# Performance work log

Measured on AMD Instinct MI355X. Metric: run time of the kernel, lower is better.

Reference implementation:

```python
import jax, jax.numpy as jnp
import numpy as np

LAMBDA_SCR = 0.015
LAMBDA_IFD = 0.015


def setup_inputs() -> dict:
    key = jax.random.key(0)
    k = jax.random.split(key, 5)
    pred = jax.random.normal(k[0], (32, 1000), dtype=jnp.float32)
    feat0 = jax.random.normal(k[1], (32, 64, 128, 128), dtype=jnp.float32)
    feat1 = jax.random.normal(k[2], (32, 128, 64, 64), dtype=jnp.float32)
    feat2 = jax.random.normal(k[3], (32, 256, 32, 32), dtype=jnp.float32)  # teacher
    target = jax.random.randint(k[4], (32,), 0, 1000, dtype=jnp.int64)
    return {"pred": pred, "feat0": feat0, "feat1": feat1, "feat2": feat2, "target": target}


def _adaptive_avg_pool2d(x, out_hw):
    # Exact-multiple adaptive average pool (matches torch for integer ratios).
    B, C, H, W = x.shape
    Ho, Wo = out_hw
    if Ho >= H:
        x = jnp.repeat(x, Ho // H, axis=2)  # replication upsample
    else:
        x = x.reshape(B, C, Ho, H // Ho, W).mean(axis=3)
    if Wo >= W:
        x = jnp.repeat(x, Wo // W, axis=3)
    else:
        x = x.reshape(B, C, x.shape[2], Wo, W // Wo).mean(axis=4)
    return x


def _random_channel_selection(feat, target_channels, key):
    C = feat.shape[1]
    if C == target_channels:
        return feat
    idx = jax.random.permutation(key, C)[:target_channels]
    return feat[:, idx, :, :]


def _ifd_loss(feat):
    B, C, H, W = feat.shape
    if C < 2:
        return jnp.float32(0.0)
    # L2 norm per channel -> descending sort of channel indices
    norms = jnp.linalg.norm(feat.reshape(B, C, H * W), axis=-1)  # [B, C]
    idx = jnp.argsort(-norms, axis=1)                            # [B, C]
    half = C // 2
    strong = jnp.take_along_axis(feat, idx[:, :half, None, None], axis=1)
    weak = jnp.take_along_axis(feat, idx[:, half:2 * half, None, None], axis=1)
    A_strong = jax.nn.sigmoid(strong.mean(axis=1))  # [B, H, W]
    A_weak = jax.nn.sigmoid(weak.mean(axis=1))
    # sum_b mean_hw(diff^2) / B == mean over all elements
    return jnp.mean((A_weak - jax.lax.stop_gradient(A_strong)) ** 2)


def reference(pred, feat0, feat1, feat2, target):
    logp = jax.nn.log_softmax(pred, axis=-1)
    l_main = -jnp.mean(jnp.take_along_axis(logp, target[:, None], axis=1))

    features = [feat0, feat1, feat2]
    teacher = features[-1]
    students = features[:-1]

    sel_key = jax.random.key(42)  # fixed keys stand in for torch.randperm
    l_scr = jnp.float32(0.0)
    for i, student in enumerate(students):
        t_down = _adaptive_avg_pool2d(teacher, student.shape[2:])
        min_C = min(teacher.shape[1], student.shape[1])
        ks, kt = jax.random.split(jax.random.fold_in(sel_key, i))
        s_aligned = _random_channel_selection(student, min_C, ks)
        t_aligned = _random_channel_selection(t_down, min_C, kt)
        l_scr = l_scr + jnp.mean((s_aligned - jax.lax.stop_gradient(t_aligned)) ** 2)
    l_scr = l_scr / len(students)

    l_ifd = jnp.float32(0.0)
    for feat in features:
        l_ifd = l_ifd + _ifd_loss(feat)
    l_ifd = l_ifd / len(features)

    total = l_main + LAMBDA_SCR * l_scr + LAMBDA_IFD * l_ifd
    return (total, l_main, l_scr, l_ifd)
```

## Files before the change

### kernel.cpp

```cpp
#include <hip/hip_runtime.h>
#include <stdint.h>
#include <math.h>

#define NB 32

__device__ __forceinline__ void tf_block(uint32_t k0, uint32_t k1, uint32_t& x0, uint32_t& x1) {
  uint32_t k2 = 0x1BD11BDAu ^ k0 ^ k1;
  x0 += k0; x1 += k1;
#define TFR(r) { x0 += x1; x1 = (x1 << r) | (x1 >> (32 - r)); x1 ^= x0; }
  TFR(13) TFR(15) TFR(26) TFR(6)
  x0 += k1; x1 += k2 + 1u;
  TFR(17) TFR(29) TFR(16) TFR(24)
  x0 += k2; x1 += k0 + 2u;
  TFR(13) TFR(15) TFR(26) TFR(6)
  x0 += k0; x1 += k1 + 3u;
  TFR(17) TFR(29) TFR(16) TFR(24)
  x0 += k1; x1 += k2 + 4u;
  TFR(13) TFR(15) TFR(26) TFR(6)
  x0 += k2; x1 += k0 + 5u;
#undef TFR
}

__device__ __forceinline__ float sigmoidf(float x) { return 1.0f / (1.0f + expf(-x)); }

__device__ __forceinline__ float block_reduce(float v, float* red) {
  __syncthreads();
  int lane = threadIdx.x & 63, wv = threadIdx.x >> 6;
  for (int o = 32; o > 0; o >>= 1) v += __shfl_down(v, o, 64);
  if (lane == 0) red[wv] = v;
  __syncthreads();
  float r = 0.f;
  if (threadIdx.x == 0) r = red[0] + red[1] + red[2] + red[3];
  return r;
}

__global__ __launch_bounds__(256) void k0_perm(int* idx0, int* idx1, float* ws) {
  __shared__ uint32_t sub[2][2];
  __shared__ uint32_t bits[2][256];
  int t = threadIdx.x;
  for (int i = t; i < 384; i += 256) ws[i] = 0.0f;
  if (t == 0) {
    for (int i = 0; i < 2; ++i) {
      uint32_t f0 = 0u, f1 = (uint32_t)i;
      tf_block(0u, 42u, f0, f1);
      uint32_t a0 = 0u, a1 = 2u; tf_block(f0, f1, a0, a1);
      uint32_t b0 = 1u, b1 = 3u; tf_block(f0, f1, b0, b1);
      uint32_t kt0 = a1, kt1 = b1;
      uint32_t c0 = 0u, c1 = 2u; tf_block(kt0, kt1, c0, c1);
      uint32_t d0 = 1u, d1 = 3u; tf_block(kt0, kt1, d0, d1);
      sub[i][0] = c1; sub[i][1] = d1;
    }
  }
  __syncthreads();
  if (t < 128) {
    for (int i = 0; i < 2; ++i) {
      uint32_t x0 = (uint32_t)t, x1 = (uint32_t)(t + 128);
      tf_block(sub[i][0], sub[i][1], x0, x1);
      bits[i][t] = x0; bits[i][t + 128] = x1;
    }
  }
  __syncthreads();
  for (int i = 0; i < 2; ++i) {
    uint32_t mine = bits[i][t];
    int rank = 0;
    for (int k = 0; k < 256; ++k) {
      uint32_t v = bits[i][k];
      rank += (v < mine) || (v == mine && k < t);
    }
    int lim = (i == 0) ? 64 : 128;
    if (rank < lim) { (i == 0 ? idx0 : idx1)[rank] = t; }
  }
}

template<int C, int HW, int LOGW, int SHIFT, bool STUDENT>
__device__ __forceinline__ void pass1_work(const float* __restrict__ feat,
                                           const float* __restrict__ teacher,
                                           const int* __restrict__ tidx,
                                           float* __restrict__ normsq,
                                           float* __restrict__ scr_slots,
                                           int bc, float* tpl, float* red) {
  if constexpr (STUDENT) {
    int b = bc / C, c = bc % C;
    int tc = tidx[c];
    ((float4*)tpl)[threadIdx.x] =
        ((const float4*)(teacher + ((size_t)b * 256 + tc) * 1024))[threadIdx.x];
    __syncthreads();
  }
  const float4* plane = (const float4*)(feat + (size_t)bc * HW);
  float ssq = 0.f, scr = 0.f;
  for (int p = threadIdx.x; p < HW / 4; p += 256) {
    float4 v = plane[p];
    ssq += v.x * v.x + v.y * v.y + v.z * v.z + v.w * v.w;
    if constexpr (STUDENT) {
      int pix = p * 4;
      int h = pix >> LOGW;
      int w = pix & ((1 << LOGW) - 1);
      int th = h >> SHIFT;
      if constexpr (SHIFT == 2) {
        float tv = tpl[th * 32 + (w >> 2)];
        float dx = v.x - tv, dy = v.y - tv, dz = v.z - tv, dw = v.w - tv;
        scr += dx * dx + dy * dy + dz * dz + dw * dw;
      } else {
        int tw = w >> 1;
        float t0 = tpl[th * 32 + tw], t1 = tpl[th * 32 + tw + 1];
        float dx = v.x - t0, dy = v.y - t0, dz = v.z - t1, dw = v.w - t1;
        scr += dx * dx + dy * dy + dz * dz + dw * dw;
      }
    }
  }
  float r = block_reduce(ssq, red);
  if (threadIdx.x == 0) normsq[bc] = r;
  if constexpr (STUDENT) {
    float r2 = block_reduce(scr, red);
    if (threadIdx.x == 0) atomicAdd(&scr_slots[bc & 63], r2);
  }
}

__global__ __launch_bounds__(256) void k1_pass1(
    const float* __restrict__ f0, const float* __restrict__ f1, const float* __restrict__ f2,
    const int* __restrict__ idx0, const int* __restrict__ idx1,
    float* __restrict__ ns0, float* __restrict__ ns1, float* __restrict__ ns2,
    float* __restrict__ scr0_s, float* __restrict__ scr1_s) {
  __shared__ float tpl[1024];
  __shared__ float red[8];
  int bid = blockIdx.x;
  if (bid < 2048)       pass1_work<64, 16384, 7, 2, true >(f0, f2, idx0, ns0, scr0_s, bid,        tpl, red);
  else if (bid < 6144)  pass1_work<128, 4096, 6, 1, true >(f1, f2, idx1, ns1, scr1_s, bid - 2048, tpl, red);
  else                  pass1_work<256, 1024, 5, 0, false>(f2, nullptr, nullptr, ns2, nullptr, bid - 6144, tpl, red);
}

template<int C>
__device__ __forceinline__ void rank_work(const float* __restrict__ normsq,
                                          float* __restrict__ flags, int b, float* nm) {
  for (int c = threadIdx.x; c < C; c += 256) nm[c] = sqrtf(normsq[b * C + c]);
  __syncthreads();
  for (int c = threadIdx.x; c < C; c += 256) {
    float mine = nm[c];
    int rank = 0;
    for (int k = 0; k < C; ++k) {
      float v = nm[k];
      rank += (v > mine) || (v == mine && k < c);
    }
    flags[b * C + c] = (rank < C / 2) ? 1.0f : 0.0f;
  }
}

__device__ __forceinline__ void main_work(const float* __restrict__ pred,
                                          const int* __restrict__ target,
                                          float* acc, int b, float* sh) {
  int t = threadIdx.x;
  const float* row = pred + b * 1000;
  float m = -INFINITY;
  for (int j = t; j < 1000; j += 256) m = fmaxf(m, row[j]);
  sh[t] = m; __syncthreads();
  for (int s = 128; s > 0; s >>= 1) { if (t < s) sh[t] = fmaxf(sh[t], sh[t + s]); __syncthreads(); }
  m = sh[0]; __syncthreads();
  float e = 0.f;
  for (int j = t; j < 1000; j += 256) e += expf(row[j] - m);
  sh[t] = e; __syncthreads();
  for (int s = 128; s > 0; s >>= 1) { if (t < s) sh[t] += sh[t + s]; __syncthreads(); }
  if (t == 0) atomicAdd(acc, (logf(sh[0]) + m - row[target[b]]) * (1.0f / 32.0f));
}

__global__ __launch_bounds__(256) void k2_rank_main(
    const float* __restrict__ ns0, const float* __restrict__ ns1, const float* __restrict__ ns2,
    float* __restrict__ fl0, float* __restrict__ fl1, float* __restrict__ fl2,
    const float* __restrict__ pred, const int* __restrict__ target, float* main_acc) {
  __shared__ float sh[256];
  int bid = blockIdx.x;
  if (bid < 32)       rank_work<64 >(ns0, fl0, bid,      sh);
  else if (bid < 64)  rank_work<128>(ns1, fl1, bid - 32, sh);
  else if (bid < 96)  rank_work<256>(ns2, fl2, bid - 64, sh);
  else                main_work(pred, target, main_acc, bid - 96, sh);
}

template<int C, int HW>
__device__ __forceinline__ void pass2_vec4_work(const float* __restrict__ feat,
                                                const float* __restrict__ flags,
                                                float* __restrict__ slots, float inv_half,
                                                int bid, float* fl, float* red) {
  const int nchunk = HW / 1024;
  int b = bid / nchunk, chunk = bid % nchunk;
  for (int c = threadIdx.x; c < C; c += 256) fl[c] = flags[b * C + c];
  __syncthreads();
  const float* base = feat + (size_t)b * C * HW + (size_t)chunk * 1024;
  float4 tot = {0, 0, 0, 0}, str = {0, 0, 0, 0};
  for (int c = 0; c < C; ++c) {
    float4 v = ((const float4*)(base + (size_t)c * HW))[threadIdx.x];
    float f = fl[c];
    tot.x += v.x; tot.y += v.y; tot.z += v.z; tot.w += v.w;
    str.x = fmaf(v.x, f, str.x); str.y = fmaf(v.y, f, str.y);
    str.z = fmaf(v.z, f, str.z); str.w = fmaf(v.w, f, str.w);
  }
  float s = 0.f, d;
  d = sigmoidf((tot.x - str.x) * inv_half) - sigmoidf(str.x * inv_half); s += d * d;
  d = sigmoidf((tot.y - str.y) * inv_half) - sigmoidf(str.y * inv_half); s += d * d;
  d = sigmoidf((tot.z - str.z) * inv_half) - sigmoidf(str.z * inv_half); s += d * d;
  d = sigmoidf((tot.w - str.w) * inv_half) - sigmoidf(str.w * inv_half); s += d * d;
  float r = block_reduce(s, red);
  if (threadIdx.x == 0) atomicAdd(&slots[bid & 63], r);
}

__device__ __forceinline__ void pass2_feat2_work(const float* __restrict__ feat,
                                                 const float* __restrict__ flags,
                                                 float* __restrict__ slots, int bid,
                                                 float* fl, float* stot, float* sstr, float* red) {
  int b = bid >> 5, h = bid & 31;
  fl[threadIdx.x] = flags[b * 256 + threadIdx.x];
  __syncthreads();
  int w = threadIdx.x & 31;
  int cl = threadIdx.x >> 5;
  const float* base = feat + (size_t)b * 256 * 1024 + h * 32 + w;
  float tot = 0.f, str = 0.f;
  for (int cg = 0; cg < 32; ++cg) {
    int c = cg * 8 + cl;
    float v = base[(size_t)c * 1024];
    tot += v; str = fmaf(v, fl[c], str);
  }
  stot[threadIdx.x] = tot; sstr[threadIdx.x] = str;
  __syncthreads();
  float s = 0.f;
  if (threadIdx.x < 32) {
    float T = 0.f, S = 0.f;
    for (int k = 0; k < 8; ++k) { T += stot[k * 32 + threadIdx.x]; S += sstr[k * 32 + threadIdx.x]; }
    const float ih = 1.0f / 128.0f;
    float d = sigmoidf((T - S) * ih) - sigmoidf(S * ih);
    s = d * d;
  }
  float r = block_reduce(s, red);
  if (threadIdx.x == 0) atomicAdd(&slots[bid & 63], r);
}

__global__ __launch_bounds__(256) void k3_pass2(
    const float* __restrict__ f0, const float* __restrict__ f1, const float* __restrict__ f2,
    const float* __restrict__ fl0, const float* __restrict__ fl1, const float* __restrict__ fl2,
    float* __restrict__ ifd0_s, float* __restrict__ ifd1_s, float* __restrict__ ifd2_s) {
  __shared__ float fl[256];
  __shared__ float s1[256];
  __shared__ float s2[256];
  __shared__ float red[8];
  int bid = blockIdx.x;
  if (bid < 512)      pass2_vec4_work<64, 16384>(f0, fl0, ifd0_s, 1.0f / 32.0f, bid, fl, red);
  else if (bid < 640) pass2_vec4_work<128, 4096>(f1, fl1, ifd1_s, 1.0f / 64.0f, bid - 512, fl, red);
  else                pass2_feat2_work(f2, fl2, ifd2_s, bid - 640, fl, s1, s2, red);
}

__global__ void k4_finalize(const float* __restrict__ ws, float* __restrict__ out) {
  float scr0 = 0.f, scr1 = 0.f, ifd0 = 0.f, ifd1 = 0.f, ifd2 = 0.f;
  for (int i = 0; i < 64; ++i) {
    scr0 += ws[i];       scr1 += ws[64 + i];
    ifd0 += ws[128 + i]; ifd1 += ws[192 + i]; ifd2 += ws[256 + i];
  }
  float l_main = ws[320];
  scr0 *= (1.0f / (32.0f * 64.0f * 128.0f * 128.0f));
  scr1 *= (1.0f / (32.0f * 128.0f * 64.0f * 64.0f));
  float l_scr = 0.5f * (scr0 + scr1);
  ifd0 *= (1.0f / (32.0f * 128.0f * 128.0f));
  ifd1 *= (1.0f / (32.0f * 64.0f * 64.0f));
  ifd2 *= (1.0f / (32.0f * 32.0f * 32.0f));
  float l_ifd = (ifd0 + ifd1 + ifd2) * (1.0f / 3.0f);
  float total = l_main + 0.015f * l_scr + 0.015f * l_ifd;
  out[0] = total; out[1] = l_main; out[2] = l_scr; out[3] = l_ifd;
}

extern "C" void kernel_launch(void* const* d_in, const int* in_sizes, int n_in,
                              void* d_out, int out_size, void* d_ws, size_t ws_size,
                              hipStream_t stream) {
  (void)in_sizes; (void)n_in; (void)out_size; (void)ws_size;
  const float* pred   = (const float*)d_in[0];
  const float* feat0  = (const float*)d_in[1];
  const float* feat1  = (const float*)d_in[2];
  const float* feat2  = (const float*)d_in[3];
  const int*   target = (const int*)d_in[4];
  float* out = (float*)d_out;

  float* ws = (float*)d_ws;
  float* scr0_s = ws;
  float* scr1_s = ws + 64;
  float* ifd0_s = ws + 128;
  float* ifd1_s = ws + 192;
  float* ifd2_s = ws + 256;
  float* main_a = ws + 320;
  int*   idx0 = (int*)(ws + 384);
  int*   idx1 = idx0 + 64;
  float* ns0  = (float*)(idx1 + 128);
  float* ns1  = ns0 + 2048;
  float* ns2  = ns1 + 4096;
  float* fl0  = ns2 + 8192;
  float* fl1  = fl0 + 2048;
  float* fl2  = fl1 + 4096;

  k0_perm<<<1, 256, 0, stream>>>(idx0, idx1, ws);
  k1_pass1<<<14336, 256, 0, stream>>>(feat0, feat1, feat2, idx0, idx1, ns0, ns1, ns2, scr0_s, scr1_s);
  k2_rank_main<<<128, 256, 0, stream>>>(ns0, ns1, ns2, fl0, fl1, fl2, pred, target, main_a);
  k3_pass2<<<1664, 256, 0, stream>>>(feat0, feat1, feat2, fl0, fl1, fl2, ifd0_s, ifd1_s, ifd2_s);
  k4_finalize<<<1, 1, 0, stream>>>(ws, out);
}
```

Measured before the change: 337.0 us.

## Assign per-wave work units and replace block reductions with wave reductions

The norm/SCR pass and the IFD pass now give each 64-lane wave its own plane or chunk for the smaller feature maps, so one 256-thread block covers four units and the grids shrink. Block-level reductions, with their two barriers and shared-memory round trip, become wave shuffles plus a single barrier or none, and loops get fixed trip counts with unrolling. The aim is to cut barrier and launch overhead and raise memory-level parallelism on these bandwidth-bound passes. The trade-off is more atomics per block and a larger shared-memory footprint, which can lower occupancy.

New measurement: 339.1 us. No clear change (+0.6%).

```diff
diff --git a/kernel.cpp b/kernel.cpp
--- a/kernel.cpp
+++ b/kernel.cpp
@@ -23,15 +23,9 @@
 
 __device__ __forceinline__ float sigmoidf(float x) { return 1.0f / (1.0f + expf(-x)); }
 
-__device__ __forceinline__ float block_reduce(float v, float* red) {
-  __syncthreads();
-  int lane = threadIdx.x & 63, wv = threadIdx.x >> 6;
+__device__ __forceinline__ float wave_reduce(float v) {
   for (int o = 32; o > 0; o >>= 1) v += __shfl_down(v, o, 64);
-  if (lane == 0) red[wv] = v;
-  __syncthreads();
-  float r = 0.f;
-  if (threadIdx.x == 0) r = red[0] + red[1] + red[2] + red[3];
-  return r;
+  return v;
 }
 
 __global__ __launch_bounds__(256) void k0_perm(int* idx0, int* idx1, float* ws) {
@@ -72,61 +66,83 @@
   }
 }
 
-template<int C, int HW, int LOGW, int SHIFT, bool STUDENT>
-__device__ __forceinline__ void pass1_work(const float* __restrict__ feat,
-                                           const float* __restrict__ teacher,
-                                           const int* __restrict__ tidx,
-                                           float* __restrict__ normsq,
-                                           float* __restrict__ scr_slots,
-                                           int bc, float* tpl, float* red) {
-  if constexpr (STUDENT) {
-    int b = bc / C, c = bc % C;
-    int tc = tidx[c];
-    ((float4*)tpl)[threadIdx.x] =
-        ((const float4*)(teacher + ((size_t)b * 256 + tc) * 1024))[threadIdx.x];
-    __syncthreads();
-  }
-  const float4* plane = (const float4*)(feat + (size_t)bc * HW);
-  float ssq = 0.f, scr = 0.f;
-  for (int p = threadIdx.x; p < HW / 4; p += 256) {
-    float4 v = plane[p];
-    ssq += v.x * v.x + v.y * v.y + v.z * v.z + v.w * v.w;
-    if constexpr (STUDENT) {
-      int pix = p * 4;
-      int h = pix >> LOGW;
-      int w = pix & ((1 << LOGW) - 1);
-      int th = h >> SHIFT;
-      if constexpr (SHIFT == 2) {
-        float tv = tpl[th * 32 + (w >> 2)];
-        float dx = v.x - tv, dy = v.y - tv, dz = v.z - tv, dw = v.w - tv;
-        scr += dx * dx + dy * dy + dz * dz + dw * dw;
-      } else {
-        int tw = w >> 1;
-        float t0 = tpl[th * 32 + tw], t1 = tpl[th * 32 + tw + 1];
-        float dx = v.x - t0, dy = v.y - t0, dz = v.z - t1, dw = v.w - t1;
-        scr += dx * dx + dy * dy + dz * dz + dw * dw;
-      }
-    }
-  }
-  float r = block_reduce(ssq, red);
-  if (threadIdx.x == 0) normsq[bc] = r;
-  if constexpr (STUDENT) {
-    float r2 = block_reduce(scr, red);
-    if (threadIdx.x == 0) atomicAdd(&scr_slots[bc & 63], r2);
-  }
-}
-
 __global__ __launch_bounds__(256) void k1_pass1(
     const float* __restrict__ f0, const float* __restrict__ f1, const float* __restrict__ f2,
     const int* __restrict__ idx0, const int* __restrict__ idx1,
     float* __restrict__ ns0, float* __restrict__ ns1, float* __restrict__ ns2,
     float* __restrict__ scr0_s, float* __restrict__ scr1_s) {
-  __shared__ float tpl[1024];
+  __shared__ float tpl[4096];
   __shared__ float red[8];
   int bid = blockIdx.x;
-  if (bid < 2048)       pass1_work<64, 16384, 7, 2, true >(f0, f2, idx0, ns0, scr0_s, bid,        tpl, red);
-  else if (bid < 6144)  pass1_work<128, 4096, 6, 1, true >(f1, f2, idx1, ns1, scr1_s, bid - 2048, tpl, red);
-  else                  pass1_work<256, 1024, 5, 0, false>(f2, nullptr, nullptr, ns2, nullptr, bid - 6144, tpl, red);
+  int lane = threadIdx.x & 63, wv = threadIdx.x >> 6;
+  if (bid < 2048) {
+    int b = bid >> 6, c = bid & 63;
+    int tc = idx0[c];
+    ((float4*)tpl)[threadIdx.x] = ((const float4*)(f2 + ((size_t)b * 256 + tc) * 1024))[threadIdx.x];
+    __syncthreads();
+    const float4* plane = (const float4*)(f0 + (size_t)bid * 16384);
+    float ssq = 0.f, scr = 0.f;
+#pragma unroll 8
+    for (int it = 0; it < 16; ++it) {
+      int p = (wv * 16 + it) * 64 + lane;
+      float4 v = plane[p];
+      int pix = p * 4, h = pix >> 7, w = pix & 127;
+      float tv = tpl[(h >> 2) * 32 + (w >> 2)];
+      ssq += v.x * v.x + v.y * v.y + v.z * v.z + v.w * v.w;
+      float dx = v.x - tv, dy = v.y - tv, dz = v.z - tv, dw = v.w - tv;
+      scr += dx * dx + dy * dy + dz * dz + dw * dw;
+    }
+    ssq = wave_reduce(ssq); scr = wave_reduce(scr);
+    if (lane == 0) { red[wv] = ssq; red[4 + wv] = scr; }
+    __syncthreads();
+    if (threadIdx.x == 0) {
+      ns0[bid] = red[0] + red[1] + red[2] + red[3];
+      atomicAdd(&scr0_s[bid & 63], red[4] + red[5] + red[6] + red[7]);
+    }
+  } else if (bid < 3072) {
+    int unit = ((bid - 2048) << 2) + wv;
+    int b = unit >> 7, c = unit & 127;
+    int tc = idx1[c];
+    const float4* tp = (const float4*)(f2 + ((size_t)b * 256 + tc) * 1024);
+#pragma unroll
+    for (int it = 0; it < 4; ++it)
+      ((float4*)tpl)[(wv << 8) + it * 64 + lane] = tp[it * 64 + lane];
+    __syncthreads();
+    const float* mytpl = tpl + (wv << 10);
+    const float4* plane = (const float4*)(f1 + (size_t)unit * 4096);
+    float ssq = 0.f, scr = 0.f;
+#pragma unroll 8
+    for (int it = 0; it < 16; ++it) {
+      int p = it * 64 + lane;
+      float4 v = plane[p];
+      int pix = p * 4, h = pix >> 6, w = pix & 63;
+      int tb = (h >> 1) * 32 + (w >> 1);
+      float t0 = mytpl[tb], t1 = mytpl[tb + 1];
+      ssq += v.x * v.x + v.y * v.y + v.z * v.z + v.w * v.w;
+      float dx = v.x - t0, dy = v.y - t0, dz = v.z - t1, dw = v.w - t1;
+      scr += dx * dx + dy * dy + dz * dz + dw * dw;
+    }
+    ssq = wave_reduce(ssq); scr = wave_reduce(scr);
+    if (lane == 0) {
+      ns1[unit] = ssq;
+      atomicAdd(&scr1_s[unit & 63], scr);
+    }
+  } else {
+    int u4 = ((bid - 3072) << 2) + wv;
+    int p0 = u4 << 2;
+#pragma unroll
+    for (int j = 0; j < 4; ++j) {
+      const float4* plane = (const float4*)(f2 + (size_t)(p0 + j) * 1024);
+      float ssq = 0.f;
+#pragma unroll
+      for (int it = 0; it < 4; ++it) {
+        float4 v = plane[it * 64 + lane];
+        ssq += v.x * v.x + v.y * v.y + v.z * v.z + v.w * v.w;
+      }
+      ssq = wave_reduce(ssq);
+      if (lane == 0) ns2[p0 + j] = ssq;
+    }
+  }
 }
 
 template<int C>
@@ -174,75 +190,78 @@
   else                main_work(pred, target, main_acc, bid - 96, sh);
 }
 
-template<int C, int HW>
-__device__ __forceinline__ void pass2_vec4_work(const float* __restrict__ feat,
-                                                const float* __restrict__ flags,
-                                                float* __restrict__ slots, float inv_half,
-                                                int bid, float* fl, float* red) {
-  const int nchunk = HW / 1024;
-  int b = bid / nchunk, chunk = bid % nchunk;
-  for (int c = threadIdx.x; c < C; c += 256) fl[c] = flags[b * C + c];
-  __syncthreads();
-  const float* base = feat + (size_t)b * C * HW + (size_t)chunk * 1024;
-  float4 tot = {0, 0, 0, 0}, str = {0, 0, 0, 0};
-  for (int c = 0; c < C; ++c) {
-    float4 v = ((const float4*)(base + (size_t)c * HW))[threadIdx.x];
-    float f = fl[c];
-    tot.x += v.x; tot.y += v.y; tot.z += v.z; tot.w += v.w;
-    str.x = fmaf(v.x, f, str.x); str.y = fmaf(v.y, f, str.y);
-    str.z = fmaf(v.z, f, str.z); str.w = fmaf(v.w, f, str.w);
-  }
-  float s = 0.f, d;
-  d = sigmoidf((tot.x - str.x) * inv_half) - sigmoidf(str.x * inv_half); s += d * d;
-  d = sigmoidf((tot.y - str.y) * inv_half) - sigmoidf(str.y * inv_half); s += d * d;
-  d = sigmoidf((tot.z - str.z) * inv_half) - sigmoidf(str.z * inv_half); s += d * d;
-  d = sigmoidf((tot.w - str.w) * inv_half) - sigmoidf(str.w * inv_half); s += d * d;
-  float r = block_reduce(s, red);
-  if (threadIdx.x == 0) atomicAdd(&slots[bid & 63], r);
-}
-
-__device__ __forceinline__ void pass2_feat2_work(const float* __restrict__ feat,
-                                                 const float* __restrict__ flags,
-                                                 float* __restrict__ slots, int bid,
-                                                 float* fl, float* stot, float* sstr, float* red) {
-  int b = bid >> 5, h = bid & 31;
-  fl[threadIdx.x] = flags[b * 256 + threadIdx.x];
-  __syncthreads();
-  int w = threadIdx.x & 31;
-  int cl = threadIdx.x >> 5;
-  const float* base = feat + (size_t)b * 256 * 1024 + h * 32 + w;
-  float tot = 0.f, str = 0.f;
-  for (int cg = 0; cg < 32; ++cg) {
-    int c = cg * 8 + cl;
-    float v = base[(size_t)c * 1024];
-    tot += v; str = fmaf(v, fl[c], str);
-  }
-  stot[threadIdx.x] = tot; sstr[threadIdx.x] = str;
-  __syncthreads();
-  float s = 0.f;
-  if (threadIdx.x < 32) {
-    float T = 0.f, S = 0.f;
-    for (int k = 0; k < 8; ++k) { T += stot[k * 32 + threadIdx.x]; S += sstr[k * 32 + threadIdx.x]; }
-    const float ih = 1.0f / 128.0f;
-    float d = sigmoidf((T - S) * ih) - sigmoidf(S * ih);
-    s = d * d;
-  }
-  float r = block_reduce(s, red);
-  if (threadIdx.x == 0) atomicAdd(&slots[bid & 63], r);
-}
-
 __global__ __launch_bounds__(256) void k3_pass2(
     const float* __restrict__ f0, const float* __restrict__ f1, const float* __restrict__ f2,
     const float* __restrict__ fl0, const float* __restrict__ fl1, const float* __restrict__ fl2,
     float* __restrict__ ifd0_s, float* __restrict__ ifd1_s, float* __restrict__ ifd2_s) {
-  __shared__ float fl[256];
-  __shared__ float s1[256];
-  __shared__ float s2[256];
-  __shared__ float red[8];
+  __shared__ float fls[1024];
   int bid = blockIdx.x;
-  if (bid < 512)      pass2_vec4_work<64, 16384>(f0, fl0, ifd0_s, 1.0f / 32.0f, bid, fl, red);
-  else if (bid < 640) pass2_vec4_work<128, 4096>(f1, fl1, ifd1_s, 1.0f / 64.0f, bid - 512, fl, red);
-  else                pass2_feat2_work(f2, fl2, ifd2_s, bid - 640, fl, s1, s2, red);
+  int lane = threadIdx.x & 63, wv = threadIdx.x >> 6;
+  if (bid < 512) {
+    int unit = (bid << 2) + wv;
+    int b = unit >> 6, chunk = unit & 63;
+    float* fl = fls + (wv << 8);
+    fl[lane] = fl0[(b << 6) + lane];
+    const float* base = f0 + (size_t)b * 64 * 16384 + (size_t)chunk * 256;
+    float4 tot = {0, 0, 0, 0}, str = {0, 0, 0, 0};
+#pragma unroll 8
+    for (int c = 0; c < 64; ++c) {
+      float4 v = ((const float4*)(base + (size_t)c * 16384))[lane];
+      float f = fl[c];
+      tot.x += v.x; tot.y += v.y; tot.z += v.z; tot.w += v.w;
+      str.x = fmaf(v.x, f, str.x); str.y = fmaf(v.y, f, str.y);
+      str.z = fmaf(v.z, f, str.z); str.w = fmaf(v.w, f, str.w);
+    }
+    const float ih = 1.0f / 32.0f;
+    float s = 0.f, d;
+    d = sigmoidf((tot.x - str.x) * ih) - sigmoidf(str.x * ih); s += d * d;
+    d = sigmoidf((tot.y - str.y) * ih) - sigmoidf(str.y * ih); s += d * d;
+    d = sigmoidf((tot.z - str.z) * ih) - sigmoidf(str.z * ih); s += d * d;
+    d = sigmoidf((tot.w - str.w) * ih) - sigmoidf(str.w * ih); s += d * d;
+    s = wave_reduce(s);
+    if (lane == 0) atomicAdd(&ifd0_s[unit & 63], s);
+  } else if (bid < 640) {
+    int unit = ((bid - 512) << 2) + wv;
+    int b = unit >> 4, chunk = unit & 15;
+    float* fl = fls + (wv << 8);
+    fl[lane] = fl1[(b << 7) + lane];
+    fl[64 + lane] = fl1[(b << 7) + 64 + lane];
+    const float* base = f1 + (size_t)b * 128 * 4096 + (size_t)chunk * 256;
+    float4 tot = {0, 0, 0, 0}, str = {0, 0, 0, 0};
+#pragma unroll 8
+    for (int c = 0; c < 128; ++c) {
+      float4 v = ((const float4*)(base + (size_t)c * 4096))[lane];
+      float f = fl[c];
+      tot.x += v.x; tot.y += v.y; tot.z += v.z; tot.w += v.w;
+      str.x = fmaf(v.x, f, str.x); str.y = fmaf(v.y, f, str.y);
+      str.z = fmaf(v.z, f, str.z); str.w = fmaf(v.w, f, str.w);
+    }
+    const float ih = 1.0f / 64.0f;
+    float s = 0.f, d;
+    d = sigmoidf((tot.x - str.x) * ih) - sigmoidf(str.x * ih); s += d * d;
+    d = sigmoidf((tot.y - str.y) * ih) - sigmoidf(str.y * ih); s += d * d;
+    d = sigmoidf((tot.z - str.z) * ih) - sigmoidf(str.z * ih); s += d * d;
+    d = sigmoidf((tot.w - str.w) * ih) - sigmoidf(str.w * ih); s += d * d;
+    s = wave_reduce(s);
+    if (lane == 0) atomicAdd(&ifd1_s[unit & 63], s);
+  } else {
+    int unit = ((bid - 640) << 2) + wv;
+    int b = unit >> 4, chunk = unit & 15;
+    float* fl = fls + (wv << 8);
+#pragma unroll
+    for (int k = 0; k < 4; ++k) fl[k * 64 + lane] = fl2[(b << 8) + k * 64 + lane];
+    const float* base = f2 + (size_t)b * 256 * 1024 + (size_t)chunk * 64 + lane;
+    float tot = 0.f, str = 0.f;
+#pragma unroll 8
+    for (int c = 0; c < 256; ++c) {
+      float v = base[(size_t)c << 10];
+      tot += v; str = fmaf(v, fl[c], str);
+    }
+    const float ih = 1.0f / 128.0f;
+    float d = sigmoidf((tot - str) * ih) - sigmoidf(str * ih);
+    float s = wave_reduce(d * d);
+    if (lane == 0) atomicAdd(&ifd2_s[unit & 63], s);
+  }
 }
 
 __global__ void k4_finalize(const float* __restrict__ ws, float* __restrict__ out) {
@@ -291,8 +310,8 @@
   float* fl2  = fl1 + 4096;
 
   k0_perm<<<1, 256, 0, stream>>>(idx0, idx1, ws);
-  k1_pass1<<<14336, 256, 0, stream>>>(feat0, feat1, feat2, idx0, idx1, ns0, ns1, ns2, scr0_s, scr1_s);
+  k1_pass1<<<3584, 256, 0, stream>>>(feat0, feat1, feat2, idx0, idx1, ns0, ns1, ns2, scr0_s, scr1_s);
   k2_rank_main<<<128, 256, 0, stream>>>(ns0, ns1, ns2, fl0, fl1, fl2, pred, target, main_a);
-  k3_pass2<<<1664, 256, 0, stream>>>(feat0, feat1, feat2, fl0, fl1, fl2, ifd0_s, ifd1_s, ifd2_s);
+  k3_pass2<<<768, 256, 0, stream>>>(feat0, feat1, feat2, fl0, fl1, fl2, ifd0_s, ifd1_s, ifd2_s);
   k4_finalize<<<1, 1, 0, stream>>>(ws, out);
 }
```
